# Kernel optimization log

Hardware: AMD Instinct MI355X
Metric: run time of the kernel (lower is better)

The kernel has to match this reference:

```python
import jax, jax.numpy as jnp
import numpy as np
from jax import lax

N_NODES = 100000
N_EDGES = 600000  # even: edges stored as consecutive reverse pairs
NODE_F = 64
EDGE_F = 16
EDGE_H = 128
NODE_H = 128
NUM_STEPS = 6


def setup_inputs() -> dict:
    key = jax.random.key(0)
    ks = jax.random.split(key, 16)
    # paired reverse edges: edge 2k is (src,dst), edge 2k+1 is (dst,src)
    src = jax.random.randint(ks[0], (N_EDGES // 2,), 0, N_NODES, dtype=jnp.int32)
    dst = jax.random.randint(ks[1], (N_EDGES // 2,), 0, N_NODES, dtype=jnp.int32)
    from_nodes = jnp.stack([src, dst], axis=1).reshape(-1)
    to_nodes = jnp.stack([dst, src], axis=1).reshape(-1)
    edges = jnp.stack([from_nodes, to_nodes], axis=0)
    return {
        "node_features": jax.random.normal(ks[2], (N_NODES, NODE_F), jnp.float32),
        "edge_features": jax.random.normal(ks[3], (N_EDGES, EDGE_F), jnp.float32),
        "edge_hiddens": jnp.zeros((N_EDGES, EDGE_H), jnp.float32),
        "edges": edges,
        "W1_w": jax.random.normal(ks[4], (NODE_F, EDGE_H), jnp.float32) / np.sqrt(NODE_F),
        "W1_b": jnp.zeros((EDGE_H,), jnp.float32),
        "W2_w": jax.random.normal(ks[5], (EDGE_F, EDGE_H), jnp.float32) / np.sqrt(EDGE_F),
        "W2_b": jnp.zeros((EDGE_H,), jnp.float32),
        "W3_w": jax.random.normal(ks[6], (EDGE_H, EDGE_H), jnp.float32) / np.sqrt(EDGE_H),
        "W3_b": jnp.zeros((EDGE_H,), jnp.float32),
        "U1_w": jax.random.normal(ks[7], (NODE_F, NODE_H), jnp.float32) / np.sqrt(NODE_F),
        "U1_b": jnp.zeros((NODE_H,), jnp.float32),
        "U2_w": jax.random.normal(ks[8], (EDGE_H, NODE_H), jnp.float32) / np.sqrt(EDGE_H),
        "U2_b": jnp.zeros((NODE_H,), jnp.float32),
    }


def reference(node_features, edge_features, edge_hiddens, edges,
              W1_w, W1_b, W2_w, W2_b, W3_w, W3_b, U1_w, U1_b, U2_w, U2_b):
    from_nodes = edges[0]
    to_nodes = edges[1]
    n_edges = edges.shape[1]
    # backlink of edge i is its reverse pair: even i -> i+1, odd i -> i-1
    idx = jnp.arange(n_edges)
    backlink = idx + ((idx + 1) % 2) * 2 - 1

    # loop-invariant terms
    W1_x_u = (node_features @ W1_w + W1_b)[from_nodes]     # [E, EH]
    W2_x_uv = edge_features @ W2_w + W2_b                  # [E, EH]

    def step(h, _):
        # sum edge hiddens by source node, gather back per-edge, drop backlink
        s = jax.ops.segment_sum(h, from_nodes, num_segments=N_NODES)  # [N, EH]
        wu = s[from_nodes] - h[backlink]                               # [E, EH]
        h_new = jax.nn.relu(W1_x_u + W2_x_uv + (wu @ W3_w + W3_b))
        return h_new, None

    edge_h, _ = lax.scan(step, edge_hiddens, None, length=NUM_STEPS)

    U1_x_u = node_features @ U1_w + U1_b                   # [N, NH]
    U2_vu = edge_h @ U2_w + U2_b                           # [E, NH]
    agg = jax.ops.segment_sum(U2_vu, to_nodes, num_segments=N_NODES)
    node_hiddens = jax.nn.relu(U1_x_u + agg)               # [N, NH]
    return node_hiddens
```

## Files before the change

### kernel.cpp

```cpp
#include <hip/hip_runtime.h>
#include <hip/hip_bf16.h>

#define N_NODES 100000
#define N_EDGES 600000
#define SCAN_BLOCKS ((N_NODES + 255) / 256)

typedef __bf16 bf16;
typedef __bf16 bf16x2 __attribute__((ext_vector_type(2)));
typedef __bf16 bf16x4 __attribute__((ext_vector_type(4)));
typedef __bf16 bf16x8 __attribute__((ext_vector_type(8)));
typedef float f32x4 __attribute__((ext_vector_type(4)));

__global__ void deg_hist(const int* __restrict__ from, int* __restrict__ deg, int E) {
    int e = blockIdx.x * blockDim.x + threadIdx.x;
    if (e < E) atomicAdd(&deg[from[e]], 1);
}

__global__ __launch_bounds__(256) void block_sums(
    const int* __restrict__ deg, int* __restrict__ bsum)
{
    __shared__ int s[256];
    int i = blockIdx.x * 256 + threadIdx.x;
    s[threadIdx.x] = (i < N_NODES) ? deg[i] : 0;
    __syncthreads();
    for (int st = 128; st > 0; st >>= 1) {
        if (threadIdx.x < st) s[threadIdx.x] += s[threadIdx.x + st];
        __syncthreads();
    }
    if (threadIdx.x == 0) bsum[blockIdx.x] = s[0];
}

__global__ __launch_bounds__(256) void scan_partials(
    const int* __restrict__ bsum, int* __restrict__ bpref, int* __restrict__ off)
{
    __shared__ int s[SCAN_BLOCKS];
    for (int i = threadIdx.x; i < SCAN_BLOCKS; i += 256) s[i] = bsum[i];
    __syncthreads();
    if (threadIdx.x == 0) {
        int run = 0;
        for (int i = 0; i < SCAN_BLOCKS; i++) { int t = s[i]; s[i] = run; run += t; }
        off[N_NODES] = run;
    }
    __syncthreads();
    for (int i = threadIdx.x; i < SCAN_BLOCKS; i += 256) bpref[i] = s[i];
}

__global__ __launch_bounds__(256) void block_scan(
    const int* __restrict__ deg, const int* __restrict__ bpref,
    int* __restrict__ off, int* __restrict__ cursor)
{
    __shared__ int s[256];
    int i = blockIdx.x * 256 + threadIdx.x;
    int v = (i < N_NODES) ? deg[i] : 0;
    s[threadIdx.x] = v;
    __syncthreads();
    for (int st = 1; st < 256; st <<= 1) {
        int x = (threadIdx.x >= st) ? s[threadIdx.x - st] : 0;
        __syncthreads();
        s[threadIdx.x] += x;
        __syncthreads();
    }
    if (i < N_NODES) {
        int o = bpref[blockIdx.x] + s[threadIdx.x] - v;
        off[i] = o;
        cursor[i] = o;
    }
}

__global__ void scatter_csr(const int* __restrict__ from, int* __restrict__ cursor,
                            int* __restrict__ se, int* __restrict__ rank, int E) {
    int e = blockIdx.x * blockDim.x + threadIdx.x;
    if (e < E) {
        int p = atomicAdd(&cursor[from[e]], 1);
        se[p] = e;
        rank[e] = p;
    }
}

__global__ void make_maps(const int* __restrict__ se, const int* __restrict__ from,
                          const int* __restrict__ rank,
                          int* __restrict__ fromP, int* __restrict__ backP, int E) {
    int i = blockIdx.x * blockDim.x + threadIdx.x;
    if (i < E) {
        int e = se[i];
        fromP[i] = from[e];
        backP[i] = rank[e ^ 1];
    }
}

__global__ __launch_bounds__(256) void node_gemm(
    const float* __restrict__ A, const float* __restrict__ B,
    const float* __restrict__ bias, float* __restrict__ C, int M)
{
    __shared__ float As[16][65];
    __shared__ float Bs[16][128];
    int row0 = blockIdx.x * 64;
    int tid = threadIdx.x;
    int tx = tid & 15, ty = tid >> 4;
    float acc[4][8];
    #pragma unroll
    for (int i = 0; i < 4; i++)
        #pragma unroll
        for (int j = 0; j < 8; j++) acc[i][j] = 0.f;

    for (int kk = 0; kk < 64; kk += 16) {
        int m  = tid >> 2;
        int k4 = (tid & 3) * 4;
        float4 v = make_float4(0.f, 0.f, 0.f, 0.f);
        if (row0 + m < M)
            v = *(const float4*)(A + (size_t)(row0 + m) * 64 + kk + k4);
        As[k4 + 0][m] = v.x; As[k4 + 1][m] = v.y;
        As[k4 + 2][m] = v.z; As[k4 + 3][m] = v.w;
        #pragma unroll
        for (int t = 0; t < 2; t++) {
            int id = tid + t * 256;
            int k = id >> 5, n4 = (id & 31) * 4;
            *(float4*)(&Bs[k][n4]) = *(const float4*)(B + (size_t)(kk + k) * 128 + n4);
        }
        __syncthreads();
        #pragma unroll
        for (int k = 0; k < 16; k++) {
            float a[4], b[8];
            #pragma unroll
            for (int i = 0; i < 4; i++) a[i] = As[k][ty * 4 + i];
            #pragma unroll
            for (int j = 0; j < 8; j++) b[j] = Bs[k][tx + j * 16];
            #pragma unroll
            for (int i = 0; i < 4; i++)
                #pragma unroll
                for (int j = 0; j < 8; j++) acc[i][j] += a[i] * b[j];
        }
        __syncthreads();
    }
    #pragma unroll
    for (int i = 0; i < 4; i++) {
        int r = row0 + ty * 4 + i;
        if (r < M) {
            #pragma unroll
            for (int j = 0; j < 8; j++) {
                int c = tx + j * 16;
                C[(size_t)r * 128 + c] = acc[i][j] + bias[c];
            }
        }
    }
}

__global__ __launch_bounds__(256) void base_sorted(
    const float* __restrict__ nodeW1, const int* __restrict__ fromP,
    const int* __restrict__ se, const float* __restrict__ ef,
    const float* __restrict__ W2, const float* __restrict__ W2b,
    const float* __restrict__ W3b, bf16* __restrict__ baseP)
{
    int tid = threadIdx.x;
    int c0 = (tid & 31) * 4;
    int sub = tid >> 5;
    float4 w[16];
    #pragma unroll
    for (int k = 0; k < 16; k++) w[k] = *(const float4*)(W2 + k * 128 + c0);
    float4 bias;
    {
        float4 a = *(const float4*)(W2b + c0);
        float4 b = *(const float4*)(W3b + c0);
        bias = make_float4(a.x + b.x, a.y + b.y, a.z + b.z, a.w + b.w);
    }
    #pragma unroll 1
    for (int it = 0; it < 64; ++it) {
        int i = blockIdx.x * 512 + it * 8 + sub;
        if (i >= N_EDGES) break;
        const float* efr = ef + (size_t)se[i] * 16;
        float4 nv = *(const float4*)(nodeW1 + (size_t)fromP[i] * 128 + c0);
        float4 acc = make_float4(bias.x + nv.x, bias.y + nv.y,
                                 bias.z + nv.z, bias.w + nv.w);
        #pragma unroll
        for (int k = 0; k < 16; k++) {
            float s = efr[k];
            acc.x += s * w[k].x; acc.y += s * w[k].y;
            acc.z += s * w[k].z; acc.w += s * w[k].w;
        }
        bf16x4 o;
        o[0] = (bf16)acc.x; o[1] = (bf16)acc.y; o[2] = (bf16)acc.z; o[3] = (bf16)acc.w;
        *(bf16x4*)(baseP + (size_t)i * 128 + c0) = o;
    }
}

__global__ __launch_bounds__(256) void prep_weights(
    const float* __restrict__ W3, const float* __restrict__ U2,
    bf16* __restrict__ W3T, bf16* __restrict__ U2T)
{
    int i = blockIdx.x * 256 + threadIdx.x;
    if (i < 128 * 128) {
        int k = i >> 7, n = i & 127;
        W3T[n * 128 + k] = (bf16)W3[k * 128 + n];
        U2T[n * 128 + k] = (bf16)U2[k * 128 + n];
    }
}

__global__ __launch_bounds__(256) void edge_mfma_v5(
    const bf16* __restrict__ baseP, const bf16* __restrict__ gBP,
    const bf16* __restrict__ S, const int* __restrict__ fromP,
    const int* __restrict__ backP, const bf16* __restrict__ BT,
    bf16* __restrict__ gout, int fused, int scatter)
{
    __shared__ bf16 Bsw[128 * 128];
    int tid = threadIdx.x;

    #pragma unroll
    for (int t = 0; t < 8; t++) {
        int c = tid + t * 256;
        int cmr = c & 15;
        int cq  = (c >> 4) & 3;
        int ckt = (c >> 6) & 3;
        int cn  = c >> 8;
        int brow = cn * 16 + cmr;
        int bcol = ckt * 32 + cq * 8;
        *(bf16x8*)&Bsw[(size_t)c * 8] =
            *(const bf16x8*)(BT + (size_t)brow * 128 + bcol);
    }
    __syncthreads();

    int wave = tid >> 6, lane = tid & 63;
    int quad = lane >> 4, mr = lane & 15;

    #pragma unroll 1
    for (int it = 0; it < 4; ++it) {
        int i0 = blockIdx.x * 256 + wave * 64 + it * 16;
        if (i0 >= N_EDGES) break;
        int i = i0 + mr;

        bf16x8 afr[4];
        if (!fused) {
            #pragma unroll
            for (int kt = 0; kt < 4; kt++) {
                bf16x8 bb = *(const bf16x8*)(baseP + (size_t)i * 128 + kt * 32 + quad * 8);
                #pragma unroll
                for (int j = 0; j < 8; j++)
                    afr[kt][j] = (bf16)fmaxf((float)bb[j], 0.f);
            }
        } else {
            const bf16* sr = S   + (size_t)fromP[i] * 128;
            const bf16* gr = gBP + (size_t)i * 128;
            #pragma unroll
            for (int kt = 0; kt < 4; kt++) {
                int c = kt * 32 + quad * 8;
                bf16x8 bb = *(const bf16x8*)(baseP + (size_t)i * 128 + c);
                bf16x8 gg = *(const bf16x8*)(gr + c);
                bf16x8 ss = *(const bf16x8*)(sr + c);
                #pragma unroll
                for (int j = 0; j < 8; j++) {
                    float v = (float)bb[j] + (float)ss[j] - (float)gg[j];
                    afr[kt][j] = (bf16)fmaxf(v, 0.f);
                }
            }
        }

        f32x4 acc[8];
        #pragma unroll
        for (int n = 0; n < 8; n++) acc[n] = (f32x4){0.f, 0.f, 0.f, 0.f};
        #pragma unroll
        for (int kt = 0; kt < 4; kt++) {
            #pragma unroll
            for (int n = 0; n < 8; n++) {
                bf16x8 b = *(const bf16x8*)&Bsw[(size_t)(((n * 4 + kt) * 64) + lane) * 8];
                acc[n] = __builtin_amdgcn_mfma_f32_16x16x32_bf16(afr[kt], b, acc[n], 0, 0, 0);
            }
        }

        int rbase4 = i0 + quad * 4;
        int orow[4];
        #pragma unroll
        for (int reg = 0; reg < 4; reg++)
            orow[reg] = scatter ? backP[rbase4 + reg] : (rbase4 + reg);

        #pragma unroll
        for (int np = 0; np < 4; np++) {
            int n0 = np * 2;
            #pragma unroll
            for (int reg = 0; reg < 4; reg++) {
                float v0 = acc[n0][reg], v1 = acc[n0 + 1][reg];
                float o0 = __shfl_xor(v0, 1);
                float o1 = __shfl_xor(v1, 1);
                bf16x2 pk;
                int colb;
                if ((mr & 1) == 0) {
                    pk[0] = (bf16)v0; pk[1] = (bf16)o0;
                    colb = n0 * 16 + mr;
                } else {
                    pk[0] = (bf16)o1; pk[1] = (bf16)v1;
                    colb = (n0 + 1) * 16 + (mr ^ 1);
                }
                *(bf16x2*)(gout + (size_t)orow[reg] * 128 + colb) = pk;
            }
        }
    }
}

__global__ __launch_bounds__(256) void segsum_scatter(
    const bf16* __restrict__ g, const int* __restrict__ backP,
    const int* __restrict__ off, bf16* __restrict__ S,
    bf16* __restrict__ gBPout)
{
    int n = blockIdx.x * 4 + (threadIdx.x >> 6);
    if (n >= N_NODES) return;
    int lane = threadIdx.x & 63;
    int o0 = off[n], o1 = off[n + 1];
    float a0 = 0.f, a1 = 0.f;
    for (int p = o0; p < o1; ++p) {
        bf16x2 v = *(const bf16x2*)(g + (size_t)p * 128 + lane * 2);
        a0 += (float)v[0];
        a1 += (float)v[1];
        int q = backP[p];
        *(bf16x2*)(gBPout + (size_t)q * 128 + lane * 2) = v;
    }
    bf16x2 o; o[0] = (bf16)a0; o[1] = (bf16)a1;
    *(bf16x2*)(S + (size_t)n * 128 + lane * 2) = o;
}

__global__ __launch_bounds__(256) void final_out_stream(
    const bf16* __restrict__ X, const int* __restrict__ off,
    const float* __restrict__ U1x, const float* __restrict__ U2b,
    float* __restrict__ out)
{
    int n = blockIdx.x * 4 + (threadIdx.x >> 6);
    if (n >= N_NODES) return;
    int lane = threadIdx.x & 63;
    int o0 = off[n], o1 = off[n + 1];
    float a0 = 0.f, a1 = 0.f;
    for (int p = o0; p < o1; ++p) {
        bf16x2 v = *(const bf16x2*)(X + (size_t)p * 128 + lane * 2);
        a0 += (float)v[0];
        a1 += (float)v[1];
    }
    float d = (float)(o1 - o0);
    float2 u = *(const float2*)(U1x + (size_t)n * 128 + lane * 2);
    float2 b = *(const float2*)(U2b + lane * 2);
    float r0 = fmaxf(u.x + a0 + d * b.x, 0.f);
    float r1 = fmaxf(u.y + a1 + d * b.y, 0.f);
    *(float2*)(out + (size_t)n * 128 + lane * 2) = make_float2(r0, r1);
}

extern "C" void kernel_launch(void* const* d_in, const int* in_sizes, int n_in,
                              void* d_out, int out_size, void* d_ws, size_t ws_size,
                              hipStream_t stream) {
    const float* nf  = (const float*)d_in[0];
    const float* ef  = (const float*)d_in[1];
    const int* edges = (const int*)d_in[3];
    const int* from  = edges;
    const float* W1w = (const float*)d_in[4];
    const float* W1b = (const float*)d_in[5];
    const float* W2w = (const float*)d_in[6];
    const float* W2b = (const float*)d_in[7];
    const float* W3w = (const float*)d_in[8];
    const float* W3b = (const float*)d_in[9];
    const float* U1w = (const float*)d_in[10];
    const float* U1b = (const float*)d_in[11];
    const float* U2w = (const float*)d_in[12];
    const float* U2b = (const float*)d_in[13];
    float* out = (float*)d_out;

    const size_t NODE_MAT = (size_t)N_NODES * 128;
    const size_t EDGE_MAT = (size_t)N_EDGES * 128;
    char* w = (char*)d_ws;
    float* nodeW1 = (float*)w; w += NODE_MAT * 4;
    bf16*  S      = (bf16*)w;  w += NODE_MAT * 2;
    bf16*  baseP  = (bf16*)w;  w += EDGE_MAT * 2;
    bf16*  G      = (bf16*)w;  w += EDGE_MAT * 2;
    bf16*  GBP    = (bf16*)w;  w += EDGE_MAT * 2;
    bf16*  W3T    = (bf16*)w;  w += 128 * 128 * 2;
    bf16*  U2T    = (bf16*)w;  w += 128 * 128 * 2;
    int*   deg    = (int*)w;   w += (size_t)N_NODES * 4;
    int*   off    = (int*)w;   w += (size_t)(N_NODES + 1) * 4;
    int*   cursor = (int*)w;   w += (size_t)N_NODES * 4;
    int*   bsum   = (int*)w;   w += (size_t)SCAN_BLOCKS * 4;
    int*   bpref  = (int*)w;   w += (size_t)SCAN_BLOCKS * 4;
    int*   se     = (int*)w;   w += (size_t)N_EDGES * 4;
    int*   rank   = (int*)w;   w += (size_t)N_EDGES * 4;
    int*   fromP  = (int*)w;   w += (size_t)N_EDGES * 4;
    int*   backP  = (int*)w;   w += (size_t)N_EDGES * 4;

    hipMemsetAsync(deg, 0, (size_t)N_NODES * 4, stream);
    deg_hist<<<(N_EDGES + 255) / 256, 256, 0, stream>>>(from, deg, N_EDGES);
    block_sums<<<SCAN_BLOCKS, 256, 0, stream>>>(deg, bsum);
    scan_partials<<<1, 256, 0, stream>>>(bsum, bpref, off);
    block_scan<<<SCAN_BLOCKS, 256, 0, stream>>>(deg, bpref, off, cursor);
    scatter_csr<<<(N_EDGES + 255) / 256, 256, 0, stream>>>(from, cursor, se, rank, N_EDGES);
    make_maps<<<(N_EDGES + 255) / 256, 256, 0, stream>>>(se, from, rank, fromP, backP, N_EDGES);

    prep_weights<<<(128 * 128 + 255) / 256, 256, 0, stream>>>(W3w, U2w, W3T, U2T);
    node_gemm<<<(N_NODES + 63) / 64, 256, 0, stream>>>(nf, W1w, W1b, nodeW1, N_NODES);
    base_sorted<<<(N_EDGES + 511) / 512, 256, 0, stream>>>(
        nodeW1, fromP, se, ef, W2w, W2b, W3b, baseP);

    const int EGRID = (N_EDGES + 255) / 256;
    const int SGRID = (N_NODES + 3) / 4;

    edge_mfma_v5<<<EGRID, 256, 0, stream>>>(
        baseP, GBP, S, fromP, backP, W3T, G, 0, 0);
    segsum_scatter<<<SGRID, 256, 0, stream>>>(G, backP, off, S, GBP);
    for (int it = 1; it < 5; ++it) {
        edge_mfma_v5<<<EGRID, 256, 0, stream>>>(
            baseP, GBP, S, fromP, backP, W3T, G, 1, 0);
        segsum_scatter<<<SGRID, 256, 0, stream>>>(G, backP, off, S, GBP);
    }
    edge_mfma_v5<<<EGRID, 256, 0, stream>>>(
        baseP, GBP, S, fromP, backP, U2T, G, 1, 1);

    node_gemm<<<(N_NODES + 63) / 64, 256, 0, stream>>>(nf, U1w, U1b, nodeW1, N_NODES);
    final_out_stream<<<SGRID, 256, 0, stream>>>(G, off, nodeW1, U2b, out);
}
```

Baseline: 1.815 ms.

## Move backlink scatter from segment-sum kernel into edge MFMA epilogue with ping-pong buffers

The edge GEMM kernel now writes each output row twice: once in CSR order for the segment sum and once scattered to its backlink position in a separate buffer. The segment-sum kernel becomes a pure streaming reduction with no scatter writes. Two backlink buffers alternate between steps so the kernel never reads and writes the same buffer in one pass. This removes the per-edge backP lookup from the segment kernel. The cost is extra global write traffic and a larger workspace.

New measurement: 1.876 ms. 1.03x slower.

```diff
diff --git a/kernel.cpp b/kernel.cpp
--- a/kernel.cpp
+++ b/kernel.cpp
@@ -195,11 +195,12 @@
     }
 }
 
-__global__ __launch_bounds__(256) void edge_mfma_v5(
-    const bf16* __restrict__ baseP, const bf16* __restrict__ gBP,
+__global__ __launch_bounds__(256) void edge_mfma_v7(
+    const bf16* __restrict__ baseP, const bf16* __restrict__ gin,
     const bf16* __restrict__ S, const int* __restrict__ fromP,
     const int* __restrict__ backP, const bf16* __restrict__ BT,
-    bf16* __restrict__ gout, int fused, int scatter)
+    bf16* __restrict__ gout, bf16* __restrict__ goutB,
+    int fused, int writeG)
 {
     __shared__ bf16 Bsw[128 * 128];
     int tid = threadIdx.x;
@@ -238,7 +239,7 @@
             }
         } else {
             const bf16* sr = S   + (size_t)fromP[i] * 128;
-            const bf16* gr = gBP + (size_t)i * 128;
+            const bf16* gr = gin + (size_t)i * 128;
             #pragma unroll
             for (int kt = 0; kt < 4; kt++) {
                 int c = kt * 32 + quad * 8;
@@ -266,10 +267,8 @@
         }
 
         int rbase4 = i0 + quad * 4;
-        int orow[4];
-        #pragma unroll
-        for (int reg = 0; reg < 4; reg++)
-            orow[reg] = scatter ? backP[rbase4 + reg] : (rbase4 + reg);
+        int4 br4 = *(const int4*)(backP + rbase4);
+        int brows[4] = {br4.x, br4.y, br4.z, br4.w};
 
         #pragma unroll
         for (int np = 0; np < 4; np++) {
@@ -288,16 +287,18 @@
                     pk[0] = (bf16)o1; pk[1] = (bf16)v1;
                     colb = (n0 + 1) * 16 + (mr ^ 1);
                 }
-                *(bf16x2*)(gout + (size_t)orow[reg] * 128 + colb) = pk;
+                if (writeG) {
+                    int row = rbase4 + reg;
+                    *(bf16x2*)(gout + (size_t)row * 128 + colb) = pk;
+                }
+                *(bf16x2*)(goutB + (size_t)brows[reg] * 128 + colb) = pk;
             }
         }
     }
 }
 
-__global__ __launch_bounds__(256) void segsum_scatter(
-    const bf16* __restrict__ g, const int* __restrict__ backP,
-    const int* __restrict__ off, bf16* __restrict__ S,
-    bf16* __restrict__ gBPout)
+__global__ __launch_bounds__(256) void segsum_stream(
+    const bf16* __restrict__ g, const int* __restrict__ off, bf16* __restrict__ S)
 {
     int n = blockIdx.x * 4 + (threadIdx.x >> 6);
     if (n >= N_NODES) return;
@@ -308,8 +309,6 @@
         bf16x2 v = *(const bf16x2*)(g + (size_t)p * 128 + lane * 2);
         a0 += (float)v[0];
         a1 += (float)v[1];
-        int q = backP[p];
-        *(bf16x2*)(gBPout + (size_t)q * 128 + lane * 2) = v;
     }
     bf16x2 o; o[0] = (bf16)a0; o[1] = (bf16)a1;
     *(bf16x2*)(S + (size_t)n * 128 + lane * 2) = o;
@@ -364,7 +363,8 @@
     bf16*  S      = (bf16*)w;  w += NODE_MAT * 2;
     bf16*  baseP  = (bf16*)w;  w += EDGE_MAT * 2;
     bf16*  G      = (bf16*)w;  w += EDGE_MAT * 2;
-    bf16*  GBP    = (bf16*)w;  w += EDGE_MAT * 2;
+    bf16*  GB0    = (bf16*)w;  w += EDGE_MAT * 2;
+    bf16*  GB1    = (bf16*)w;  w += EDGE_MAT * 2;
     bf16*  W3T    = (bf16*)w;  w += 128 * 128 * 2;
     bf16*  U2T    = (bf16*)w;  w += 128 * 128 * 2;
     int*   deg    = (int*)w;   w += (size_t)N_NODES * 4;
@@ -393,17 +393,24 @@
     const int EGRID = (N_EDGES + 255) / 256;
     const int SGRID = (N_NODES + 3) / 4;
 
-    edge_mfma_v5<<<EGRID, 256, 0, stream>>>(
-        baseP, GBP, S, fromP, backP, W3T, G, 0, 0);
-    segsum_scatter<<<SGRID, 256, 0, stream>>>(G, backP, off, S, GBP);
+    bf16* GBa = GB0;
+    bf16* GBb = GB1;
+
+    edge_mfma_v7<<<EGRID, 256, 0, stream>>>(
+        baseP, GBa, S, fromP, backP, W3T, G, GBb, 0, 1);
+    segsum_stream<<<SGRID, 256, 0, stream>>>(G, off, S);
+    { bf16* t = GBa; GBa = GBb; GBb = t; }
+
     for (int it = 1; it < 5; ++it) {
-        edge_mfma_v5<<<EGRID, 256, 0, stream>>>(
-            baseP, GBP, S, fromP, backP, W3T, G, 1, 0);
-        segsum_scatter<<<SGRID, 256, 0, stream>>>(G, backP, off, S, GBP);
-    }
-    edge_mfma_v5<<<EGRID, 256, 0, stream>>>(
-        baseP, GBP, S, fromP, backP, U2T, G, 1, 1);
+        edge_mfma_v7<<<EGRID, 256, 0, stream>>>(
+            baseP, GBa, S, fromP, backP, W3T, G, GBb, 1, 1);
+        segsum_stream<<<SGRID, 256, 0, stream>>>(G, off, S);
+        { bf16* t = GBa; GBa = GBb; GBb = t; }
+    }
+
+    edge_mfma_v7<<<EGRID, 256, 0, stream>>>(
+        baseP, GBa, S, fromP, backP, U2T, G, GBb, 1, 0);
 
     node_gemm<<<(N_NODES + 63) / 64, 256, 0, stream>>>(nf, U1w, U1b, nodeW1, N_NODES);
-    final_out_stream<<<SGRID, 256, 0, stream>>>(G, off, nodeW1, U2b, out);
-}
+    final_out_stream<<<SGRID, 256, 0, stream>>>(GBb, off, nodeW1, U2b, out);
+}
```
